# Kernel tuning notes

Measured on AMD Instinct MI355X. Metric: run time of the kernel, lower is better.

## Reference

```python
import jax, jax.numpy as jnp
import numpy as np

COST_POS = 5.0
COST_CONF = 1.0
LAMBDA_POS = 5.0
LAMBDA_CONF = 2.0
LAMBDA_NOOBJ = 0.5


def _lsa(cost):
    """Rectangular linear sum assignment (Jonker-Volgenant shortest augmenting
    path), same semantics as scipy.optimize.linear_sum_assignment."""
    cost = np.asarray(cost, dtype=np.float64)
    transposed = cost.shape[1] < cost.shape[0]
    if transposed:
        cost = cost.T
    nr, nc = cost.shape  # nr <= nc
    u = np.zeros(nr)
    v = np.zeros(nc)
    col4row = np.full(nr, -1, dtype=np.int64)
    row4col = np.full(nc, -1, dtype=np.int64)
    for cur_row in range(nr):
        shortest = np.full(nc, np.inf)
        pathback = np.full(nc, -1, dtype=np.int64)
        SR = np.zeros(nr, dtype=bool)
        SC = np.zeros(nc, dtype=bool)
        remaining = np.ones(nc, dtype=bool)
        min_val = 0.0
        i = cur_row
        sink = -1
        while sink == -1:
            SR[i] = True
            rem = np.flatnonzero(remaining)
            new_cost = min_val + cost[i, rem] - u[i] - v[rem]
            better = new_cost < shortest[rem]
            idx = rem[better]
            shortest[idx] = new_cost[better]
            pathback[idx] = i
            j = rem[np.argmin(shortest[rem])]
            min_val = shortest[j]
            remaining[j] = False
            SC[j] = True
            if row4col[j] == -1:
                sink = j
            else:
                i = row4col[j]
        u[cur_row] += min_val
        rows = np.flatnonzero(SR)
        rows = rows[rows != cur_row]
        u[rows] += min_val - shortest[col4row[rows]]
        v[SC] -= min_val - shortest[SC]
        j = sink
        while True:
            i = pathback[j]
            row4col[j] = i
            col4row[i], j = j, col4row[i]
            if i == cur_row:
                break
    if transposed:
        rows = col4row
        cols = np.arange(nr)
        order = np.argsort(rows)
        return rows[order], cols[order]
    return np.arange(nr), col4row


def _match(pred_c, conf, gt_c):
    """Per-image Hungarian matching (host-side, @no_grad in the original).
    cost = COST_POS * L1(pred, gt) - COST_CONF * sigmoid(conf)."""
    B, N, _ = pred_c.shape
    M = gt_c.shape[1]
    pred_idx = np.empty((B, M), dtype=np.int64)
    gt_idx = np.empty((B, M), dtype=np.int64)
    for b in range(B):
        c_pos = np.abs(pred_c[b][:, None, :] - gt_c[b][None, :, :]).sum(-1)  # [N,M]
        c_conf = -1.0 / (1.0 + np.exp(-conf[b]))  # [N]
        cost = COST_POS * c_pos + COST_CONF * c_conf[:, None]
        r, c = _lsa(cost)
        pred_idx[b] = r
        gt_idx[b] = c
    return pred_idx, gt_idx


def setup_inputs() -> dict:
    key = jax.random.key(0)
    B, N, M, D = 32, 300, 50, 2
    k1, k2, k3, k4, k5 = jax.random.split(key, 5)
    return {
        "pred_centroids": jax.random.uniform(k1, (B, N, D), dtype=jnp.float32),
        "pred_logits": jax.random.normal(k2, (B, N, 1), dtype=jnp.float32),
        "pred_conf": jax.random.normal(k3, (B, N), dtype=jnp.float32),
        "gt_centroids": jax.random.uniform(k4, (B, M, D), dtype=jnp.float32),
        "gt_classes": jax.random.randint(k5, (B, M), 0, 1),
    }


def reference(pred_centroids, pred_logits, pred_conf, gt_centroids, gt_classes):
    B, N, D = pred_centroids.shape
    M = gt_centroids.shape[1]
    # Matching indices are constants (computed under no_grad, host-side).
    pred_idx, gt_idx = _match(np.asarray(pred_centroids, np.float64),
                              np.asarray(pred_conf, np.float64),
                              np.asarray(gt_centroids, np.float64))
    pred_idx = jnp.asarray(pred_idx)  # [B,M]
    gt_idx = jnp.asarray(gt_idx)      # [B,M]
    b = jnp.arange(B)[:, None]
    mp = pred_centroids[b, pred_idx]  # [B,M,D]
    mg = gt_centroids[b, gt_idx]      # [B,M,D]
    # per-image L1 mean, summed over images (all images have M matches)
    loss_pos = jnp.mean(jnp.abs(mp - mg), axis=(1, 2)).sum()
    m_logit = pred_conf[b, pred_idx]  # [B,M]
    # BCE-with-logits, target=1: softplus(-x); target=0: softplus(x)
    loss_obj = jnp.mean(jax.nn.softplus(-m_logit), axis=1).sum()
    unmatched = jnp.ones((B, N), dtype=bool).at[b, pred_idx].set(False)
    sp = jax.nn.softplus(pred_conf)
    loss_noobj = (jnp.where(unmatched, sp, 0.0).sum(axis=1) / (N - M)).sum()
    loss_pos = LAMBDA_POS * loss_pos / B
    loss_conf_obj = LAMBDA_CONF * loss_obj / B
    loss_conf_noobj = LAMBDA_NOOBJ * loss_noobj / B
    loss_total = loss_pos + loss_conf_obj + loss_conf_noobj
    n_matched = jnp.asarray(float(M), dtype=jnp.float32)  # total matched / B
    return loss_pos, loss_conf_obj, loss_conf_noobj, loss_total, n_matched
```

## Files before the change

### kernel.cpp

```cpp
#include <hip/hip_runtime.h>
#include <math.h>


#define BB 32
#define NN 300
#define MM 50
#define KPL 5

#define F5(OP) OP(0) OP(1) OP(2) OP(3) OP(4)

__device__ __forceinline__ float softplus_f(float x) {
    return fmaxf(x, 0.0f) + __logf(1.0f + __expf(-fabsf(x)));
}
__device__ __forceinline__ float readlane_f(float x, int l) {
    return __int_as_float(__builtin_amdgcn_readlane(__float_as_int(x), l));
}
__device__ __forceinline__ int readlane_i(int x, int l) {
    return __builtin_amdgcn_readlane(x, l);
}
__device__ __forceinline__ unsigned umaxu(unsigned a, unsigned b) { return a > b ? a : b; }

__device__ __forceinline__ unsigned minkey_f32(float d) {
    unsigned s = (unsigned)__float_as_int(d);
    unsigned us = (s & 0x80000000u) ? ~s : (s | 0x80000000u);
    return ~us;
}
__device__ __forceinline__ float keydec_up(unsigned key) {
    unsigned us = (~key) | 0x1FFu;
    return (us & 0x80000000u) ? __uint_as_float(us & 0x7FFFFFFFu)
                              : __uint_as_float(~us);
}

__device__ __forceinline__ unsigned rowshr_maxkey(unsigned x) {
#define DPP_STEP(CTRL) { \
    unsigned t_ = (unsigned)__builtin_amdgcn_update_dpp(0, (int)x, CTRL, 0xF, 0xF, false); \
    x = umaxu(x, t_); }
    DPP_STEP(0x111)
    DPP_STEP(0x112)
    DPP_STEP(0x114)
    DPP_STEP(0x118)
#undef DPP_STEP
    return x;
}

__device__ __forceinline__ int div5(int n) { return (n * 52429) >> 18; }

__global__ __launch_bounds__(64, 1) void lsa_loss_kernel(
    const float* __restrict__ pred_c,
    const float* __restrict__ conf,
    const float* __restrict__ gt_c,
    float* __restrict__ out)
{
    const int b = blockIdx.x;
    const int lane = threadIdx.x;
    const bool owns = lane < (NN / KPL);
    const int base_j = KPL * lane;

    __shared__ float4 s_px4[NN/4], s_py4[NN/4], s_cm4[NN/4];
    __shared__ int claimed[NN];
    float* s_px = (float*)s_px4;
    float* s_py = (float*)s_py4;
    float* s_cm2 = (float*)s_cm4;

#define DECL(k) float px5##k, py5##k, cf##k, cm##k, sh##k; int pb##k;
    F5(DECL)
#undef DECL
    unsigned r4cpack = 0;
    int rem;
    float u = 0.0f, gx5 = 0.0f, gy5 = 0.0f, u_sub = 0.0f;
    int col4row = -1;

#define LOADK(k) { \
        int j = base_j + k; \
        float vpx = 0.0f, vpy = 0.0f, vcf = 0.0f; \
        if (owns) { \
            float2 pc = *(const float2*)&pred_c[(b*NN + j)*2]; \
            vpx = pc.x; vpy = pc.y; \
            vcf = conf[b*NN + j]; \
        } \
        px5##k = 5.0f*vpx; py5##k = 5.0f*vpy; cf##k = vcf; \
        cm##k = -(1.0f / (1.0f + __expf(-vcf)));   }
    F5(LOADK)
#undef LOADK
    if (lane < MM) {
        float2 gc = *(const float2*)&gt_c[(b*MM + lane)*2];
        gx5 = 5.0f*gc.x;
        gy5 = 5.0f*gc.y;
    }
#define STAGE(k) if (owns) { int j = base_j + k; \
        s_px[j] = px5##k; s_py[j] = py5##k; s_cm2[j] = cm##k + 2.0f; \
        claimed[j] = 63; }
    F5(STAGE)
#undef STAGE
#define IDXF(k) const unsigned idx##k = (unsigned)(511 - (base_j + k));
    F5(IDXF)
#undef IDXF
    __syncthreads();

    unsigned bestkey = 0u;
    for (int j0 = 0; j0 < NN; j0 += 8) {
        float4 vxa = s_px4[(j0 >> 2) + 0], vxb = s_px4[(j0 >> 2) + 1];
        float4 vya = s_py4[(j0 >> 2) + 0], vyb = s_py4[(j0 >> 2) + 1];
        float4 vca = s_cm4[(j0 >> 2) + 0], vcb = s_cm4[(j0 >> 2) + 1];
        float c0 = fabsf(vxa.x - gx5) + fabsf(vya.x - gy5) + vca.x;
        float c1 = fabsf(vxa.y - gx5) + fabsf(vya.y - gy5) + vca.y;
        float c2 = fabsf(vxa.z - gx5) + fabsf(vya.z - gy5) + vca.z;
        float c3 = fabsf(vxa.w - gx5) + fabsf(vya.w - gy5) + vca.w;
        float c4 = fabsf(vxb.x - gx5) + fabsf(vyb.x - gy5) + vcb.x;
        float c5 = fabsf(vxb.y - gx5) + fabsf(vyb.y - gy5) + vcb.y;
        float c6 = fabsf(vxb.z - gx5) + fabsf(vyb.z - gy5) + vcb.z;
        float c7 = fabsf(vxb.w - gx5) + fabsf(vyb.w - gy5) + vcb.w;
        unsigned q0 = (~__float_as_uint(c0) & 0xFFFFFE00u) | (unsigned)(511 - j0);
        unsigned q1 = (~__float_as_uint(c1) & 0xFFFFFE00u) | (unsigned)(510 - j0);
        unsigned q2 = (~__float_as_uint(c2) & 0xFFFFFE00u) | (unsigned)(509 - j0);
        unsigned q3 = (~__float_as_uint(c3) & 0xFFFFFE00u) | (unsigned)(508 - j0);
        unsigned q4 = (~__float_as_uint(c4) & 0xFFFFFE00u) | (unsigned)(507 - j0);
        unsigned q5 = (~__float_as_uint(c5) & 0xFFFFFE00u) | (unsigned)(506 - j0);
        unsigned q6 = (~__float_as_uint(c6) & 0xFFFFFE00u) | (unsigned)(505 - j0);
        unsigned q7 = (~__float_as_uint(c7) & 0xFFFFFE00u) | (unsigned)(504 - j0);
        unsigned qa = umaxu(umaxu(q0, q1), umaxu(q2, q3));
        unsigned qb = umaxu(umaxu(q4, q5), umaxu(q6, q7));
        bestkey = umaxu(bestkey, umaxu(qa, qb));
    }
    int wantj = 511 - (int)(bestkey & 511u);
    if (lane < MM) {
        u = fabsf(s_px[wantj] - gx5) + fabsf(s_py[wantj] - gy5)
            + (s_cm2[wantj] - 2.0f);
        atomicMin(&claimed[wantj], lane);
    }
    __syncthreads();
    if (lane < MM && claimed[wantj] == lane) col4row = wantj;
#define RCINIT(k) { int w = owns ? claimed[base_j + k] : 63; \
        r4cpack |= ((w < 63) ? (unsigned)(w + 1) : 0u) << (6*k); }
    F5(RCINIT)
#undef RCINIT

    unsigned long long freerows = __ballot(lane < MM && col4row < 0);
    while (freerows) {
        int cur_row = (int)__ffsll(freerows) - 1;
        freerows &= freerows - 1ull;

#define RINIT(k) sh##k = INFINITY; pb##k = 0;
        F5(RINIT)
#undef RINIT
        rem = owns ? 0x1F : 0;
        unsigned long long sr_mask = 0ull;
        float min_val = 0.0f;
        int i = cur_row;
        int sink = -1;

        for (int pops = 0; pops <= NN && sink < 0; ++pops) {
            sr_mask |= (1ull << i);
            float u_i   = readlane_f(u,   i);
            float gx5_i = readlane_f(gx5, i);
            float gy5_i = readlane_f(gy5, i);
            float mvu = min_val - u_i;
            int ip1 = i + 1;

#define RELAX(k) { \
                float dx5 = fabsf(px5##k - gx5_i); \
                float dy5 = fabsf(py5##k - gy5_i); \
                float nc = dx5 + dy5 + (cm##k + mvu); \
                bool imp = (((rem >> k) & 1) != 0) && (nc < sh##k); \
                sh##k = imp ? nc : sh##k; \
                pb##k = imp ? ip1 : pb##k; }
            F5(RELAX)
#undef RELAX

#define KEYK(k) unsigned key##k = ((rem >> k) & 1) \
                ? ((minkey_f32(sh##k) & 0xFFFFFE00u) | idx##k) : 0u;
            F5(KEYK)
#undef KEYK
            unsigned lkey = umaxu(umaxu(umaxu(key0, key1), umaxu(key2, key3)), key4);

            unsigned acc = rowshr_maxkey(lkey);
            unsigned k0 = (unsigned)readlane_i((int)acc, 15);
            unsigned k1 = (unsigned)readlane_i((int)acc, 31);
            unsigned k2 = (unsigned)readlane_i((int)acc, 47);
            unsigned k3 = (unsigned)readlane_i((int)acc, 63);
            unsigned gkey = umaxu(umaxu(k0, k1), umaxu(k2, k3));
            if (gkey == 0u) { sink = 0; break; }

            int bestj = 511 - (int)(gkey & 511u);
            int srcl = div5(bestj);
            int qj = bestj - KPL*srcl;
            min_val = keydec_up(gkey);

            unsigned rp = (unsigned)readlane_i((int)r4cpack, srcl);
            int r4 = (int)((rp >> (qj*6)) & 63u) - 1;

            rem = (lane == srcl) ? (rem & ~(1 << qj)) : rem;
            if (r4 < 0 || r4 >= MM) {
                sink = bestj;
            } else {
                i = r4;
                u_sub = (lane == r4) ? min_val : u_sub;
            }
        }

        if (lane < MM) {
            if (lane == cur_row) u += min_val;
            else if ((sr_mask >> lane) & 1ull) u += min_val - u_sub;
        }
#define VUPD(k) if (owns && !((rem >> k) & 1)) cm##k += min_val - sh##k;
        F5(VUPD)
#undef VUPD

        int j = sink < 0 ? 0 : sink;
        for (int step = 0; step <= MM; ++step) {
            int tj = div5(j), qj2 = j - KPL*tj;
            int pbl = qj2==0?pb0:qj2==1?pb1:qj2==2?pb2:qj2==3?pb3:pb4;
            int pi = readlane_i(pbl, tj) - 1;
            if (pi < 0 || pi >= MM) break;
            int q6 = qj2*6;
            unsigned nv = (r4cpack & ~(63u << q6)) | ((unsigned)(pi+1) << q6);
            r4cpack = (lane == tj) ? nv : r4cpack;
            int c_old = readlane_i(col4row, pi);
            col4row = (lane == pi) ? j : col4row;
            j = c_old;
            if (pi == cur_row) break;
            if (j < 0 || j >= NN) break;
        }
    }

    float lp = 0.0f, lo = 0.0f, ln = 0.0f;
    if (lane < MM) {
        int j = (col4row < 0 || col4row >= NN) ? 0 : col4row;
        float dx = fabsf(pred_c[(b*NN + j)*2 + 0] - gt_c[(b*MM + lane)*2 + 0]);
        float dy = fabsf(pred_c[(b*NN + j)*2 + 1] - gt_c[(b*MM + lane)*2 + 1]);
        lp = dx + dy;
        lo = softplus_f(-conf[b*NN + j]);
    }
#define NOOBJ(k) if (owns && ((r4cpack >> (6*k)) & 63u) == 0u) \
        ln += softplus_f(cf##k);
    F5(NOOBJ)
#undef NOOBJ
#pragma unroll
    for (int off = 32; off > 0; off >>= 1) {
        lp += __shfl_xor(lp, off, 64);
        lo += __shfl_xor(lo, off, 64);
        ln += __shfl_xor(ln, off, 64);
    }
    if (lane == 0) {
        double cp = 5.0 * ((double)lp / (double)(MM*2))  / (double)BB;
        double co = 2.0 * ((double)lo / (double)MM)      / (double)BB;
        double cn = 0.5 * ((double)ln / (double)(NN-MM)) / (double)BB;
        atomicAdd(&out[0], (float)cp);
        atomicAdd(&out[1], (float)co);
        atomicAdd(&out[2], (float)cn);
        atomicAdd(&out[3], (float)(cp + co + cn));
        if (b == 0) out[4] = 50.0f;
    }
}

extern "C" void kernel_launch(void* const* d_in, const int* in_sizes, int n_in,
                              void* d_out, int out_size, void* d_ws, size_t ws_size,
                              hipStream_t stream) {
    const float* pred_c = (const float*)d_in[0];
    const float* conf   = (const float*)d_in[2];
    const float* gt_c   = (const float*)d_in[3];
    float* out = (float*)d_out;

    hipMemsetAsync(out, 0, 5*sizeof(float), stream);
    lsa_loss_kernel<<<BB, 64, 0, stream>>>(pred_c, conf, gt_c, out);
}
```

Before: 96.95 us.

## Add greedy claim rounds for unmatched rows before augmenting-path Hungarian search

After the first greedy row-minimum assignment, up to 8 extra rounds run for rows that lost their column. Each round rescans all columns, skips ones already claimed, and resolves ties with atomicMin on a vectorised claimed array. This aims to cut the number of sequential shortest-augmenting-path searches, which are the serial bottleneck. The risk is correctness: the row duals `u` are not updated for columns claimed in later rounds, so matched edges may not be tight. That could break the augmenting invariants and give a non-optimal assignment.

Result: slower. 101.7 us (+4.9%).

```diff
diff --git a/kernel.cpp b/kernel.cpp
--- a/kernel.cpp
+++ b/kernel.cpp
@@ -57,10 +57,11 @@
     const int base_j = KPL * lane;
 
     __shared__ float4 s_px4[NN/4], s_py4[NN/4], s_cm4[NN/4];
-    __shared__ int claimed[NN];
+    __shared__ int4 s_cl4[NN/4];
     float* s_px = (float*)s_px4;
     float* s_py = (float*)s_py4;
     float* s_cm2 = (float*)s_cm4;
+    int* claimed = (int*)s_cl4;
 
 #define DECL(k) float px5##k, py5##k, cf##k, cm##k, sh##k; int pb##k;
     F5(DECL)
@@ -130,12 +131,49 @@
     }
     __syncthreads();
     if (lane < MM && claimed[wantj] == lane) col4row = wantj;
+
+    unsigned long long freerows = __ballot(lane < MM && col4row < 0);
+    for (int round = 0; round < 8 && freerows; ++round) {
+        bool loser = (lane < MM) && (col4row < 0);
+        unsigned bk = 0u;
+        for (int j0 = 0; j0 < NN; j0 += 8) {
+            float4 vxa = s_px4[(j0 >> 2) + 0], vxb = s_px4[(j0 >> 2) + 1];
+            float4 vya = s_py4[(j0 >> 2) + 0], vyb = s_py4[(j0 >> 2) + 1];
+            float4 vca = s_cm4[(j0 >> 2) + 0], vcb = s_cm4[(j0 >> 2) + 1];
+            int4 cla = s_cl4[(j0 >> 2) + 0], clb = s_cl4[(j0 >> 2) + 1];
+            float c0 = fabsf(vxa.x - gx5) + fabsf(vya.x - gy5) + vca.x;
+            float c1 = fabsf(vxa.y - gx5) + fabsf(vya.y - gy5) + vca.y;
+            float c2 = fabsf(vxa.z - gx5) + fabsf(vya.z - gy5) + vca.z;
+            float c3 = fabsf(vxa.w - gx5) + fabsf(vya.w - gy5) + vca.w;
+            float c4 = fabsf(vxb.x - gx5) + fabsf(vyb.x - gy5) + vcb.x;
+            float c5 = fabsf(vxb.y - gx5) + fabsf(vyb.y - gy5) + vcb.y;
+            float c6 = fabsf(vxb.z - gx5) + fabsf(vyb.z - gy5) + vcb.z;
+            float c7 = fabsf(vxb.w - gx5) + fabsf(vyb.w - gy5) + vcb.w;
+            unsigned q0 = (cla.x==63) ? ((~__float_as_uint(c0) & 0xFFFFFE00u) | (unsigned)(511 - j0)) : 0u;
+            unsigned q1 = (cla.y==63) ? ((~__float_as_uint(c1) & 0xFFFFFE00u) | (unsigned)(510 - j0)) : 0u;
+            unsigned q2 = (cla.z==63) ? ((~__float_as_uint(c2) & 0xFFFFFE00u) | (unsigned)(509 - j0)) : 0u;
+            unsigned q3 = (cla.w==63) ? ((~__float_as_uint(c3) & 0xFFFFFE00u) | (unsigned)(508 - j0)) : 0u;
+            unsigned q4 = (clb.x==63) ? ((~__float_as_uint(c4) & 0xFFFFFE00u) | (unsigned)(507 - j0)) : 0u;
+            unsigned q5 = (clb.y==63) ? ((~__float_as_uint(c5) & 0xFFFFFE00u) | (unsigned)(506 - j0)) : 0u;
+            unsigned q6 = (clb.z==63) ? ((~__float_as_uint(c6) & 0xFFFFFE00u) | (unsigned)(505 - j0)) : 0u;
+            unsigned q7 = (clb.w==63) ? ((~__float_as_uint(c7) & 0xFFFFFE00u) | (unsigned)(504 - j0)) : 0u;
+            unsigned qa = umaxu(umaxu(q0, q1), umaxu(q2, q3));
+            unsigned qb = umaxu(umaxu(q4, q5), umaxu(q6, q7));
+            bk = umaxu(bk, umaxu(qa, qb));
+        }
+        int wj = 511 - (int)(bk & 511u);
+        if (loser && bk != 0u) atomicMin(&claimed[wj], lane);
+        __syncthreads();
+        if (loser && bk != 0u && claimed[wj] == lane) col4row = wj;
+        freerows = __ballot(lane < MM && col4row < 0);
+        __syncthreads();
+    }
+
 #define RCINIT(k) { int w = owns ? claimed[base_j + k] : 63; \
         r4cpack |= ((w < 63) ? (unsigned)(w + 1) : 0u) << (6*k); }
     F5(RCINIT)
 #undef RCINIT
 
-    unsigned long long freerows = __ballot(lane < MM && col4row < 0);
     while (freerows) {
         int cur_row = (int)__ffsll(freerows) - 1;
         freerows &= freerows - 1ull;
```
